# Performance work log

Hardware: AMD Instinct MI355X
Metric: run time of the kernel (lower is better)

## Reference

```python
import jax, jax.numpy as jnp
import numpy as np

EPS = 1e-6
N_HEADS = 16
KV_HEADS = 4
HEAD_DIM = 64
N_REP = N_HEADS // KV_HEADS
N_EXPERTS = 8
TOP_K = 2


def _rms_norm(x, w):
    return x * jax.lax.rsqrt(jnp.mean(x * x, axis=-1, keepdims=True) + EPS) * w


def _apply_rope(x, fc):
    # x: (B,T,H,D); fc: (T, D//2, 2) holding (cos, sin)
    B, T, H, D = x.shape
    xr = x.reshape(B, T, H, D // 2, 2)
    f = fc.reshape(1, T, 1, D // 2, 2)
    re = xr[..., 0] * f[..., 0] - xr[..., 1] * f[..., 1]
    im = xr[..., 1] * f[..., 0] + xr[..., 0] * f[..., 1]
    return jnp.stack([re, im], axis=-1).reshape(B, T, H, D)


def _silu(x):
    return x * jax.nn.sigmoid(x)


def setup_inputs():
    key = jax.random.key(0)
    ks = jax.random.split(key, 16)
    B, T, C = 4, 1024, 1024
    IE, IS = 1024, 2048  # expert_inter_dim, shared inter_dim
    s = 0.02
    x = jax.random.normal(ks[0], (B, T, C), jnp.float32)
    inv_freq = 1.0 / (10000.0 ** (np.arange(0, HEAD_DIM, 2, dtype=np.float32) / HEAD_DIM))
    ang = np.outer(np.arange(T, dtype=np.float32), inv_freq)
    freq_cis = jnp.asarray(np.stack([np.cos(ang), np.sin(ang)], axis=-1), jnp.float32)
    causal = np.tril(np.ones((T, T), dtype=bool))
    mask = jnp.asarray(np.where(causal, 0.0, -1e9), dtype=jnp.float32).reshape(1, 1, T, T)
    window = jnp.zeros((1, 1, T, T), jnp.float32)
    return {
        "x": x,
        "freq_cis": freq_cis,
        "mask": mask,
        "window": window,
        "norm1_w": jnp.ones((C,), jnp.float32),
        "wq": jax.random.normal(ks[1], (N_HEADS * HEAD_DIM, C), jnp.float32) * s,
        "wk": jax.random.normal(ks[2], (KV_HEADS * HEAD_DIM, C), jnp.float32) * s,
        "wv": jax.random.normal(ks[3], (KV_HEADS * HEAD_DIM, C), jnp.float32) * s,
        "wo": jax.random.normal(ks[4], (C, N_HEADS * HEAD_DIM), jnp.float32) * s,
        "norm2_w": jnp.ones((C,), jnp.float32),
        "gate_w": jax.random.normal(ks[5], (N_EXPERTS, C), jnp.float32) * s,
        "exp_w1": jax.random.normal(ks[6], (N_EXPERTS, IE, C), jnp.float32) * s,
        "exp_w2": jax.random.normal(ks[7], (N_EXPERTS, IE, C), jnp.float32) * s,
        "exp_wp": jax.random.normal(ks[8], (N_EXPERTS, C, IE), jnp.float32) * s,
        "sh_w1": jax.random.normal(ks[9], (IS, C), jnp.float32) * s,
        "sh_w2": jax.random.normal(ks[10], (IS, C), jnp.float32) * s,
        "sh_wp": jax.random.normal(ks[11], (C, IS), jnp.float32) * s,
        "start_pos": 0,
    }


def reference(x, freq_cis, mask, window, norm1_w, wq, wk, wv, wo, norm2_w,
              gate_w, exp_w1, exp_w2, exp_wp, sh_w1, sh_w2, sh_wp, start_pos):
    B, T, C = x.shape
    # ---- pre-norm attention (GQA, Global mask, eval: no dropout) ----
    xn = _rms_norm(x, norm1_w)
    q = (xn @ wq.T).reshape(B, T, N_HEADS, HEAD_DIM)
    k = (xn @ wk.T).reshape(B, T, KV_HEADS, HEAD_DIM)
    v = (xn @ wv.T).reshape(B, T, KV_HEADS, HEAD_DIM)
    q = _apply_rope(q, freq_cis)
    k = _apply_rope(k, freq_cis)
    k = jnp.repeat(k, N_REP, axis=2)  # (B,T,H,D)
    v = jnp.repeat(v, N_REP, axis=2)
    scale = 1.0 / np.sqrt(HEAD_DIM).astype(np.float32)
    att = jnp.einsum("bqhd,bkhd->bhqk", q, k) * scale + mask
    p = jax.nn.softmax(att, axis=-1)
    o = jnp.einsum("bhqk,bkhd->bqhd", p, v).reshape(B, T, C)
    x = x + o @ wo.T
    # ---- pre-norm MoE FFN ----
    xn2 = _rms_norm(x, norm2_w).reshape(-1, C)  # (N,C)
    scores = xn2 @ gate_w.T                      # gate logits, returned
    probs = jax.nn.softmax(scores, axis=-1)
    top_w, top_i = jax.lax.top_k(probs, TOP_K)   # (N,K)
    # dense combine weights (N,E): zero for non-selected experts
    wfull = jnp.sum(jax.nn.one_hot(top_i, N_EXPERTS, dtype=x.dtype) * top_w[..., None], axis=1)
    h = _silu(jnp.einsum("nc,eic->eni", xn2, exp_w1)) * jnp.einsum("nc,eic->eni", xn2, exp_w2)
    ye = jnp.einsum("eni,eci->enc", h, exp_wp)   # per-expert outputs
    y = jnp.einsum("ne,enc->nc", wfull, ye)      # routed combine
    z = (_silu(xn2 @ sh_w1.T) * (xn2 @ sh_w2.T)) @ sh_wp.T  # shared expert
    out = x + (y + z).reshape(B, T, C)
    return out, scores
```

## Files before the change

### kernel.cpp

```cpp
#include <hip/hip_runtime.h>


typedef __bf16 bf16_t;
typedef __bf16 bf16x8 __attribute__((ext_vector_type(8)));
typedef __bf16 bf16x4 __attribute__((ext_vector_type(4)));
typedef float  f32x4  __attribute__((ext_vector_type(4)));

#define LQKV 1536

#define GLD16(gp, lp) __builtin_amdgcn_global_load_lds(                         \
    (const __attribute__((address_space(1))) void*)(gp),                        \
    (__attribute__((address_space(3))) void*)(lp), 16, 0, 0)

__global__ __launch_bounds__(256) void convert_k(
    const float* __restrict__ src, bf16_t* __restrict__ dst)
{
    size_t i = (size_t)blockIdx.x * 256 + threadIdx.x;
    float4 v = *((const float4*)src + i);
    bf16x4 o;
    o[0] = (bf16_t)v.x; o[1] = (bf16_t)v.y; o[2] = (bf16_t)v.z; o[3] = (bf16_t)v.w;
    *((bf16x4*)dst + i) = o;
}

struct Cvt8 {
    const float* s[8];
    bf16_t* d[8];
    int cum[9];
    int nseg;
};

__global__ __launch_bounds__(256) void convert_multi_k(Cvt8 j)
{
    int blk = blockIdx.x;
    int seg = 0;
    while (seg + 1 < j.nseg && blk >= j.cum[seg + 1]) ++seg;
    size_t i = (size_t)(blk - j.cum[seg]) * 256 + threadIdx.x;
    float4 v = *((const float4*)j.s[seg] + i);
    bf16x4 o;
    o[0] = (bf16_t)v.x; o[1] = (bf16_t)v.y; o[2] = (bf16_t)v.z; o[3] = (bf16_t)v.w;
    *((bf16x4*)j.d[seg] + i) = o;
}

__global__ __launch_bounds__(256) void gemm_bt(
    const bf16_t* __restrict__ A, const bf16_t* __restrict__ W,
    int M, int N, int K, int ldw, int mode,
    float* __restrict__ outF, bf16_t* __restrict__ outB,
    const float* __restrict__ resF, float* __restrict__ outF2)
{
    __shared__ __align__(16) bf16_t sA[128 * 64];
    __shared__ __align__(16) bf16_t sB[128 * 64];
    const int tid  = threadIdx.x;
    const int bm   = blockIdx.y * 128, bn = blockIdx.x * 128;
    const int lane = tid & 63;
    const int wv   = tid >> 6;
    const int wm   = (wv >> 1) * 64, wn = (wv & 1) * 64;
    const int lr   = lane & 15;
    const int kg   = lane >> 4;

    f32x4 acc[4][4];
    #pragma unroll
    for (int i = 0; i < 4; ++i)
        #pragma unroll
        for (int j = 0; j < 4; ++j)
            acc[i][j] = f32x4{0.f, 0.f, 0.f, 0.f};

    for (int k0 = 0; k0 < K; k0 += 64) {
        #pragma unroll
        for (int p = 0; p < 4; ++p) {
            int idx = p * 256 + tid;
            int row = idx >> 3, ch = (idx & 7) * 8;
            GLD16(A + (size_t)(bm + row) * K   + k0 + ch, sA + idx * 8);
            GLD16(W + (size_t)(bn + row) * ldw + k0 + ch, sB + idx * 8);
        }
        __syncthreads();
        #pragma unroll
        for (int ks = 0; ks < 2; ++ks) {
            bf16x8 af[4], bfr[4];
            #pragma unroll
            for (int i = 0; i < 4; ++i)
                af[i] = *(const bf16x8*)(sA + (wm + i * 16 + lr) * 64 + ks * 32 + kg * 8);
            #pragma unroll
            for (int j = 0; j < 4; ++j)
                bfr[j] = *(const bf16x8*)(sB + (wn + j * 16 + lr) * 64 + ks * 32 + kg * 8);
            #pragma unroll
            for (int i = 0; i < 4; ++i)
                #pragma unroll
                for (int j = 0; j < 4; ++j)
                    acc[i][j] = __builtin_amdgcn_mfma_f32_16x16x32_bf16(
                        af[i], bfr[j], acc[i][j], 0, 0, 0);
        }
        __syncthreads();
    }

    #pragma unroll
    for (int i = 0; i < 4; ++i) {
        #pragma unroll
        for (int j = 0; j < 4; ++j) {
            #pragma unroll
            for (int rr = 0; rr < 4; ++rr) {
                int m = bm + wm + i * 16 + kg * 4 + rr;
                int n = bn + wn + j * 16 + lr;
                size_t o = (size_t)m * N + n;
                float v = acc[i][j][rr];
                if (mode == 0)      outF[o] = v;
                else if (mode == 1) outB[o] = (bf16_t)v;
                else if (mode == 2) {
                    float r = v + resF[o];
                    outF[o] = r;
                    if (outF2) outF2[o] = r;
                } else              outF[o] += v;
            }
        }
    }
}

__global__ __launch_bounds__(256) void gemm_glu(
    const bf16_t* __restrict__ A, const bf16_t* __restrict__ W1,
    const bf16_t* __restrict__ W2, int M, int N, int K,
    bf16_t* __restrict__ out)
{
    __shared__ __align__(16) bf16_t sA[128 * 64];
    __shared__ __align__(16) bf16_t sB1[128 * 64];
    __shared__ __align__(16) bf16_t sB2[128 * 64];
    const int tid  = threadIdx.x;
    const int bm   = blockIdx.y * 128, bn = blockIdx.x * 128;
    const int lane = tid & 63;
    const int wv   = tid >> 6;
    const int wm   = (wv >> 1) * 64, wn = (wv & 1) * 64;
    const int lr   = lane & 15;
    const int kg   = lane >> 4;

    f32x4 acc1[4][4], acc2[4][4];
    #pragma unroll
    for (int i = 0; i < 4; ++i)
        #pragma unroll
        for (int j = 0; j < 4; ++j) {
            acc1[i][j] = f32x4{0.f, 0.f, 0.f, 0.f};
            acc2[i][j] = f32x4{0.f, 0.f, 0.f, 0.f};
        }

    for (int k0 = 0; k0 < K; k0 += 64) {
        #pragma unroll
        for (int p = 0; p < 4; ++p) {
            int idx = p * 256 + tid;
            int row = idx >> 3, ch = (idx & 7) * 8;
            GLD16(A  + (size_t)(bm + row) * K + k0 + ch, sA  + idx * 8);
            GLD16(W1 + (size_t)(bn + row) * K + k0 + ch, sB1 + idx * 8);
            GLD16(W2 + (size_t)(bn + row) * K + k0 + ch, sB2 + idx * 8);
        }
        __syncthreads();
        #pragma unroll
        for (int ks = 0; ks < 2; ++ks) {
            bf16x8 af[4], b1[4], b2[4];
            #pragma unroll
            for (int i = 0; i < 4; ++i)
                af[i] = *(const bf16x8*)(sA + (wm + i * 16 + lr) * 64 + ks * 32 + kg * 8);
            #pragma unroll
            for (int j = 0; j < 4; ++j) {
                b1[j] = *(const bf16x8*)(sB1 + (wn + j * 16 + lr) * 64 + ks * 32 + kg * 8);
                b2[j] = *(const bf16x8*)(sB2 + (wn + j * 16 + lr) * 64 + ks * 32 + kg * 8);
            }
            #pragma unroll
            for (int i = 0; i < 4; ++i)
                #pragma unroll
                for (int j = 0; j < 4; ++j) {
                    acc1[i][j] = __builtin_amdgcn_mfma_f32_16x16x32_bf16(
                        af[i], b1[j], acc1[i][j], 0, 0, 0);
                    acc2[i][j] = __builtin_amdgcn_mfma_f32_16x16x32_bf16(
                        af[i], b2[j], acc2[i][j], 0, 0, 0);
                }
        }
        __syncthreads();
    }

    #pragma unroll
    for (int i = 0; i < 4; ++i) {
        #pragma unroll
        for (int j = 0; j < 4; ++j) {
            #pragma unroll
            for (int rr = 0; rr < 4; ++rr) {
                int m = bm + wm + i * 16 + kg * 4 + rr;
                int n = bn + wn + j * 16 + lr;
                float v1 = acc1[i][j][rr], v2 = acc2[i][j][rr];
                out[(size_t)m * N + n] = (bf16_t)(v1 / (1.f + __expf(-v1)) * v2);
            }
        }
    }
}

__device__ __forceinline__ int seg_off(const int* cnt, int e)
{
    int r = 0;
    #pragma unroll
    for (int k = 0; k < 8; ++k) if (k < e) r += (cnt[k] + 127) & ~127;
    return r;
}

__global__ __launch_bounds__(256) void glu_gather(
    const bf16_t* __restrict__ A, const bf16_t* __restrict__ W1,
    const bf16_t* __restrict__ W2, const int* __restrict__ tok_list,
    const int* __restrict__ cnt, bf16_t* __restrict__ h)
{
    const int e = blockIdx.y >> 5, t = blockIdx.y & 31;
    const int ce = cnt[e];
    if (t * 128 >= ce) return;
    const int hbase = seg_off(cnt, e) + t * 128;
    const bf16_t* W1e = W1 + (size_t)e * 1048576;
    const bf16_t* W2e = W2 + (size_t)e * 1048576;

    __shared__ __align__(16) bf16_t sA[128 * 64];
    __shared__ __align__(16) bf16_t sB1[128 * 64];
    __shared__ __align__(16) bf16_t sB2[128 * 64];
    const int tid  = threadIdx.x;
    const int bn   = blockIdx.x * 128;
    const int lane = tid & 63;
    const int wv   = tid >> 6;
    const int wm   = (wv >> 1) * 64, wn = (wv & 1) * 64;
    const int lr   = lane & 15;
    const int kg   = lane >> 4;

    int tok4[4];
    #pragma unroll
    for (int p = 0; p < 4; ++p)
        tok4[p] = tok_list[e * 4096 + t * 128 + ((p * 256 + tid) >> 3)];

    f32x4 acc1[4][4], acc2[4][4];
    #pragma unroll
    for (int i = 0; i < 4; ++i)
        #pragma unroll
        for (int j = 0; j < 4; ++j) {
            acc1[i][j] = f32x4{0.f, 0.f, 0.f, 0.f};
            acc2[i][j] = f32x4{0.f, 0.f, 0.f, 0.f};
        }

    for (int k0 = 0; k0 < 1024; k0 += 64) {
        #pragma unroll
        for (int p = 0; p < 4; ++p) {
            int idx = p * 256 + tid;
            int row = idx >> 3, ch = (idx & 7) * 8;
            GLD16(A   + (size_t)tok4[p] * 1024 + k0 + ch,    sA  + idx * 8);
            GLD16(W1e + (size_t)(bn + row) * 1024 + k0 + ch, sB1 + idx * 8);
            GLD16(W2e + (size_t)(bn + row) * 1024 + k0 + ch, sB2 + idx * 8);
        }
        __syncthreads();
        #pragma unroll
        for (int ks = 0; ks < 2; ++ks) {
            bf16x8 af[4], b1[4], b2[4];
            #pragma unroll
            for (int i = 0; i < 4; ++i)
                af[i] = *(const bf16x8*)(sA + (wm + i * 16 + lr) * 64 + ks * 32 + kg * 8);
            #pragma unroll
            for (int j = 0; j < 4; ++j) {
                b1[j] = *(const bf16x8*)(sB1 + (wn + j * 16 + lr) * 64 + ks * 32 + kg * 8);
                b2[j] = *(const bf16x8*)(sB2 + (wn + j * 16 + lr) * 64 + ks * 32 + kg * 8);
            }
            #pragma unroll
            for (int i = 0; i < 4; ++i)
                #pragma unroll
                for (int j = 0; j < 4; ++j) {
                    acc1[i][j] = __builtin_amdgcn_mfma_f32_16x16x32_bf16(
                        af[i], b1[j], acc1[i][j], 0, 0, 0);
                    acc2[i][j] = __builtin_amdgcn_mfma_f32_16x16x32_bf16(
                        af[i], b2[j], acc2[i][j], 0, 0, 0);
                }
        }
        __syncthreads();
    }

    #pragma unroll
    for (int i = 0; i < 4; ++i) {
        #pragma unroll
        for (int j = 0; j < 4; ++j) {
            #pragma unroll
            for (int rr = 0; rr < 4; ++rr) {
                int rl = wm + i * 16 + kg * 4 + rr;
                int n  = bn + wn + j * 16 + lr;
                float v1 = acc1[i][j][rr], v2 = acc2[i][j][rr];
                h[(size_t)(hbase + rl) * 1024 + n] =
                    (bf16_t)(v1 / (1.f + __expf(-v1)) * v2);
            }
        }
    }
}

__global__ __launch_bounds__(256) void down_gather(
    const bf16_t* __restrict__ h, const bf16_t* __restrict__ Wp,
    const int* __restrict__ tok_list, const float* __restrict__ w_list,
    const int* __restrict__ cnt, float* __restrict__ out)
{
    const int e = blockIdx.y >> 5, t = blockIdx.y & 31;
    const int ce = cnt[e];
    if (t * 128 >= ce) return;
    const int hbase = seg_off(cnt, e) + t * 128;
    const bf16_t* We = Wp + (size_t)e * 1048576;

    __shared__ __align__(16) bf16_t sA[128 * 64];
    __shared__ __align__(16) bf16_t sB[128 * 64];
    const int tid  = threadIdx.x;
    const int bn   = blockIdx.x * 128;
    const int lane = tid & 63;
    const int wv   = tid >> 6;
    const int wm   = (wv >> 1) * 64, wn = (wv & 1) * 64;
    const int lr   = lane & 15;
    const int kg   = lane >> 4;

    f32x4 acc[4][4];
    #pragma unroll
    for (int i = 0; i < 4; ++i)
        #pragma unroll
        for (int j = 0; j < 4; ++j)
            acc[i][j] = f32x4{0.f, 0.f, 0.f, 0.f};

    for (int k0 = 0; k0 < 1024; k0 += 64) {
        #pragma unroll
        for (int p = 0; p < 4; ++p) {
            int idx = p * 256 + tid;
            int row = idx >> 3, ch = (idx & 7) * 8;
            GLD16(h  + (size_t)(hbase + row) * 1024 + k0 + ch, sA + idx * 8);
            GLD16(We + (size_t)(bn + row) * 1024 + k0 + ch,    sB + idx * 8);
        }
        __syncthreads();
        #pragma unroll
        for (int ks = 0; ks < 2; ++ks) {
            bf16x8 af[4], bfr[4];
            #pragma unroll
            for (int i = 0; i < 4; ++i)
                af[i] = *(const bf16x8*)(sA + (wm + i * 16 + lr) * 64 + ks * 32 + kg * 8);
            #pragma unroll
            for (int j = 0; j < 4; ++j)
                bfr[j] = *(const bf16x8*)(sB + (wn + j * 16 + lr) * 64 + ks * 32 + kg * 8);
            #pragma unroll
            for (int i = 0; i < 4; ++i)
                #pragma unroll
                for (int j = 0; j < 4; ++j)
                    acc[i][j] = __builtin_amdgcn_mfma_f32_16x16x32_bf16(
                        af[i], bfr[j], acc[i][j], 0, 0, 0);
        }
        __syncthreads();
    }

    #pragma unroll
    for (int i = 0; i < 4; ++i) {
        #pragma unroll
        for (int rr = 0; rr < 4; ++rr) {
            int g = t * 128 + wm + i * 16 + kg * 4 + rr;
            if (g < ce) {
                int   tok = tok_list[e * 4096 + g];
                float wgt = w_list[e * 4096 + g];
                #pragma unroll
                for (int j = 0; j < 4; ++j) {
                    int n = bn + wn + j * 16 + lr;
                    atomicAdd(&out[(size_t)tok * 1024 + n], wgt * acc[i][j][rr]);
                }
            }
        }
    }
}

__global__ __launch_bounds__(256) void rmsnorm_k(
    const float* __restrict__ src, const float* __restrict__ w,
    bf16_t* __restrict__ dst)
{
    const int row = blockIdx.x, tid = threadIdx.x;
    float4 t4 = *((const float4*)src + (size_t)row * 256 + tid);
    float ssum = t4.x*t4.x + t4.y*t4.y + t4.z*t4.z + t4.w*t4.w;
    #pragma unroll
    for (int off = 32; off > 0; off >>= 1) ssum += __shfl_down(ssum, off);
    __shared__ float red[4];
    if ((tid & 63) == 0) red[tid >> 6] = ssum;
    __syncthreads();
    float total = red[0] + red[1] + red[2] + red[3];
    float rms = rsqrtf(total * (1.0f / 1024.0f) + 1e-6f);
    float4 w4 = *((const float4*)w + tid);
    bf16x4 o4;
    o4[0] = (bf16_t)(t4.x * rms * w4.x);
    o4[1] = (bf16_t)(t4.y * rms * w4.y);
    o4[2] = (bf16_t)(t4.z * rms * w4.z);
    o4[3] = (bf16_t)(t4.w * rms * w4.w);
    *((bf16x4*)dst + (size_t)row * 256 + tid) = o4;
}

__global__ __launch_bounds__(256) void rmsnorm_gate_k(
    const float* __restrict__ src, const float* __restrict__ w,
    const float* __restrict__ gw, bf16_t* __restrict__ dst,
    float* __restrict__ scores, int* __restrict__ topi,
    float* __restrict__ topw)
{
    const int row = blockIdx.x, tid = threadIdx.x;
    float4 t4 = *((const float4*)src + (size_t)row * 256 + tid);
    float ssum = t4.x*t4.x + t4.y*t4.y + t4.z*t4.z + t4.w*t4.w;
    #pragma unroll
    for (int off = 32; off > 0; off >>= 1) ssum += __shfl_down(ssum, off);
    __shared__ float red[4];
    if ((tid & 63) == 0) red[tid >> 6] = ssum;
    __syncthreads();
    float total = red[0] + red[1] + red[2] + red[3];
    float rms = rsqrtf(total * (1.0f / 1024.0f) + 1e-6f);
    float4 w4 = *((const float4*)w + tid);
    float4 f4;
    f4.x = t4.x * rms * w4.x;
    f4.y = t4.y * rms * w4.y;
    f4.z = t4.z * rms * w4.z;
    f4.w = t4.w * rms * w4.w;
    bf16x4 o4;
    o4[0] = (bf16_t)f4.x; o4[1] = (bf16_t)f4.y;
    o4[2] = (bf16_t)f4.z; o4[3] = (bf16_t)f4.w;
    *((bf16x4*)dst + (size_t)row * 256 + tid) = o4;

    float a[8];
    #pragma unroll
    for (int e = 0; e < 8; ++e) {
        float4 g4 = *((const float4*)(gw + (size_t)e * 1024) + tid);
        a[e] = f4.x * g4.x + f4.y * g4.y + f4.z * g4.z + f4.w * g4.w;
    }
    #pragma unroll
    for (int e = 0; e < 8; ++e)
        #pragma unroll
        for (int off = 32; off > 0; off >>= 1) a[e] += __shfl_down(a[e], off);
    __shared__ float gred[4][8];
    if ((tid & 63) == 0)
        #pragma unroll
        for (int e = 0; e < 8; ++e) gred[tid >> 6][e] = a[e];
    __syncthreads();
    if (tid == 0) {
        float lg[8];
        #pragma unroll
        for (int e = 0; e < 8; ++e)
            lg[e] = gred[0][e] + gred[1][e] + gred[2][e] + gred[3][e];
        #pragma unroll
        for (int e = 0; e < 8; ++e) scores[(size_t)row * 8 + e] = lg[e];
        float mx = lg[0];
        #pragma unroll
        for (int e = 1; e < 8; ++e) mx = fmaxf(mx, lg[e]);
        float p[8], sum = 0.f;
        #pragma unroll
        for (int e = 0; e < 8; ++e) { p[e] = __expf(lg[e] - mx); sum += p[e]; }
        float inv = 1.0f / sum;
        #pragma unroll
        for (int e = 0; e < 8; ++e) p[e] *= inv;
        int i1 = 0;
        #pragma unroll
        for (int e = 1; e < 8; ++e) if (p[e] > p[i1]) i1 = e;
        int i2 = (i1 == 0) ? 1 : 0;
        #pragma unroll
        for (int e = 0; e < 8; ++e) if (e != i1 && p[e] > p[i2]) i2 = e;
        topi[row] = i1 | (i2 << 8);
        topw[row * 2]     = p[i1];
        topw[row * 2 + 1] = p[i2];
    }
}

__global__ __launch_bounds__(256) void build_lists_k(
    const int* __restrict__ topi, const float* __restrict__ topw,
    int* __restrict__ tok_list, float* __restrict__ w_list,
    int* __restrict__ cnt)
{
    const int e = blockIdx.x;
    const int tid = threadIdx.x, lane = tid & 63, wv = tid >> 6;
    __shared__ int wc[4];
    int base = 0;
    for (int t0 = 0; t0 < 4096; t0 += 256) {
        int tok = t0 + tid;
        int ti = topi[tok];
        int i1 = ti & 255, i2 = (ti >> 8) & 255;
        bool m = (i1 == e) || (i2 == e);
        unsigned long long b = __ballot(m);
        if (lane == 0) wc[wv] = __popcll(b);
        __syncthreads();
        int pos = base;
        #pragma unroll
        for (int k = 0; k < 4; ++k) if (k < wv) pos += wc[k];
        pos += __popcll(b & ((1ull << lane) - 1ull));
        if (m) {
            tok_list[e * 4096 + pos] = tok;
            w_list[e * 4096 + pos]   = (i1 == e) ? topw[tok * 2] : topw[tok * 2 + 1];
        }
        base += wc[0] + wc[1] + wc[2] + wc[3];
        __syncthreads();
    }
    int padded = (base + 127) & ~127;
    for (int p = base + tid; p < padded; p += 256) tok_list[e * 4096 + p] = 0;
    if (tid == 0) cnt[e] = base;
}

__global__ __launch_bounds__(256) void rope_all_k(
    bf16_t* __restrict__ qkv, const float* __restrict__ fc)
{
    int idx = blockIdx.x * 256 + threadIdx.x;
    int pr = idx & 31;
    int hn = idx >> 5;
    int h  = hn % 20;
    int n  = hn / 20;
    int tpos = n & 1023;
    const float* f = fc + ((size_t)tpos * 32 + pr) * 2;
    float c = f[0], s = f[1];
    int col = (h < 16) ? h * 64 : 1024 + (h - 16) * 64;
    size_t base = (size_t)n * LQKV + col + pr * 2;
    float x0 = (float)qkv[base], x1 = (float)qkv[base + 1];
    qkv[base]     = (bf16_t)(x0 * c - x1 * s);
    qkv[base + 1] = (bf16_t)(x1 * c + x0 * s);
}

__global__ __launch_bounds__(256) void transpose_v(
    const bf16_t* __restrict__ qkv, bf16_t* __restrict__ vt)
{
    __shared__ bf16_t tile[64][72];
    const int tt = blockIdx.x, kvh = blockIdx.y, b = blockIdx.z;
    const int tid = threadIdx.x;
    {
        int r = tid >> 2, c = (tid & 3) * 16;
        const bf16_t* src = qkv + ((size_t)(b * 1024 + tt * 64 + r)) * LQKV
                            + 1280 + kvh * 64 + c;
        bf16x8 v0 = *(const bf16x8*)src;
        bf16x8 v1 = *(const bf16x8*)(src + 8);
        *(bf16x8*)&tile[r][c] = v0;
        *(bf16x8*)&tile[r][c + 8] = v1;
    }
    __syncthreads();
    {
        int d = tid >> 2, t4 = (tid & 3) * 16;
        bf16_t* dst = vt + ((size_t)((b * 4 + kvh) * 64 + d)) * 1024 + tt * 64 + t4;
        bf16x8 o0, o1;
        #pragma unroll
        for (int u = 0; u < 8; ++u) {
            o0[u] = tile[t4 + u][d];
            o1[u] = tile[t4 + 8 + u][d];
        }
        *(bf16x8*)dst = o0;
        *(bf16x8*)(dst + 8) = o1;
    }
}

__global__ __launch_bounds__(256) void attn_mfma(
    const bf16_t* __restrict__ qkv, const bf16_t* __restrict__ vt,
    bf16_t* __restrict__ ob)
{
    const int qt = blockIdx.x, h = blockIdx.y, b = blockIdx.z;
    const int kvh = h >> 2;
    __shared__ __align__(16) bf16_t sK[64 * 64];
    __shared__ __align__(16) bf16_t sVt[64 * 64];
    __shared__ __align__(16) bf16_t sP[64 * 72];
    const int tid  = threadIdx.x;
    const int w    = tid >> 6;
    const int lane = tid & 63;
    const int lr   = lane & 15;
    const int kg   = lane >> 4;
    const int swz  = (lr & 7) << 3;

    bf16x8 qf[2];
    {
        const bf16_t* qrow = qkv + ((size_t)(b * 1024 + qt * 64 + w * 16 + lr)) * LQKV
                             + h * 64;
        qf[0] = *(const bf16x8*)(qrow + kg * 8);
        qf[1] = *(const bf16x8*)(qrow + 32 + kg * 8);
    }
    float m_run[4], l_run[4];
    f32x4 o_acc[4];
    #pragma unroll
    for (int rr = 0; rr < 4; ++rr) { m_run[rr] = -1.0e30f; l_run[rr] = 0.f; }
    #pragma unroll
    for (int dt = 0; dt < 4; ++dt) o_acc[dt] = f32x4{0.f, 0.f, 0.f, 0.f};

    for (int kt = 0; kt <= qt; ++kt) {
        #pragma unroll
        for (int p = 0; p < 2; ++p) {
            int idx = p * 256 + tid;
            int row = idx >> 3;
            int chs = ((idx & 7) * 8) ^ ((row & 7) << 3);
            GLD16(qkv + ((size_t)(b * 1024 + kt * 64 + row)) * LQKV
                      + 1024 + kvh * 64 + chs, sK + idx * 8);
            GLD16(vt + ((size_t)((b * 4 + kvh) * 64 + row)) * 1024 + kt * 64 + chs,
                  sVt + idx * 8);
        }
        __syncthreads();

        f32x4 sfr[4];
        #pragma unroll
        for (int j = 0; j < 4; ++j) {
            sfr[j] = f32x4{0.f, 0.f, 0.f, 0.f};
            #pragma unroll
            for (int ks = 0; ks < 2; ++ks) {
                bf16x8 bf = *(const bf16x8*)(sK + (j * 16 + lr) * 64 +
                                             ((ks * 32 + kg * 8) ^ swz));
                sfr[j] = __builtin_amdgcn_mfma_f32_16x16x32_bf16(qf[ks], bf, sfr[j], 0, 0, 0);
            }
        }
        const int rowg = qt * 64 + w * 16 + kg * 4;
        float mnew[4];
        #pragma unroll
        for (int rr = 0; rr < 4; ++rr) mnew[rr] = m_run[rr];
        #pragma unroll
        for (int j = 0; j < 4; ++j) {
            int colg = kt * 64 + j * 16 + lr;
            #pragma unroll
            for (int rr = 0; rr < 4; ++rr) {
                float s = sfr[j][rr] * 0.125f;
                if (colg > rowg + rr) s = -1.0e30f;
                sfr[j][rr] = s;
                mnew[rr] = fmaxf(mnew[rr], s);
            }
        }
        #pragma unroll
        for (int off = 1; off < 16; off <<= 1)
            #pragma unroll
            for (int rr = 0; rr < 4; ++rr)
                mnew[rr] = fmaxf(mnew[rr], __shfl_xor(mnew[rr], off, 64));
        float alpha[4], lpart[4];
        #pragma unroll
        for (int rr = 0; rr < 4; ++rr) {
            alpha[rr] = __expf(m_run[rr] - mnew[rr]);
            lpart[rr] = 0.f;
        }
        #pragma unroll
        for (int j = 0; j < 4; ++j)
            #pragma unroll
            for (int rr = 0; rr < 4; ++rr) {
                float p = __expf(sfr[j][rr] - mnew[rr]);
                sfr[j][rr] = p;
                lpart[rr] += p;
            }
        #pragma unroll
        for (int j = 0; j < 4; ++j)
            #pragma unroll
            for (int rr = 0; rr < 4; ++rr)
                sP[(w * 16 + kg * 4 + rr) * 72 + j * 16 + lr] = (bf16_t)sfr[j][rr];
        #pragma unroll
        for (int off = 1; off < 16; off <<= 1)
            #pragma unroll
            for (int rr = 0; rr < 4; ++rr)
                lpart[rr] += __shfl_xor(lpart[rr], off, 64);
        #pragma unroll
        for (int rr = 0; rr < 4; ++rr) {
            l_run[rr] = l_run[rr] * alpha[rr] + lpart[rr];
            m_run[rr] = mnew[rr];
        }
        #pragma unroll
        for (int dt = 0; dt < 4; ++dt)
            #pragma unroll
            for (int rr = 0; rr < 4; ++rr)
                o_acc[dt][rr] *= alpha[rr];
        #pragma unroll
        for (int ks = 0; ks < 2; ++ks) {
            bf16x8 af = *(const bf16x8*)(sP + (w * 16 + lr) * 72 + ks * 32 + kg * 8);
            #pragma unroll
            for (int dt = 0; dt < 4; ++dt) {
                bf16x8 bf = *(const bf16x8*)(sVt + (dt * 16 + lr) * 64 +
                                             ((ks * 32 + kg * 8) ^ swz));
                o_acc[dt] = __builtin_amdgcn_mfma_f32_16x16x32_bf16(af, bf, o_acc[dt], 0, 0, 0);
            }
        }
        __syncthreads();
    }

    float inv[4];
    #pragma unroll
    for (int rr = 0; rr < 4; ++rr) inv[rr] = 1.0f / l_run[rr];
    #pragma unroll
    for (int dt = 0; dt < 4; ++dt)
        #pragma unroll
        for (int rr = 0; rr < 4; ++rr) {
            int tok = qt * 64 + w * 16 + kg * 4 + rr;
            ob[((size_t)(b * 1024 + tok)) * 1024 + h * 64 + dt * 16 + lr] =
                (bf16_t)(o_acc[dt][rr] * inv[rr]);
        }
}

extern "C" void kernel_launch(void* const* d_in, const int* in_sizes, int n_in,
                              void* d_out, int out_size, void* d_ws, size_t ws_size,
                              hipStream_t stream)
{
    const float* x   = (const float*)d_in[0];
    const float* fc  = (const float*)d_in[1];
    const float* n1w = (const float*)d_in[4];
    const float* wq  = (const float*)d_in[5];
    const float* wk  = (const float*)d_in[6];
    const float* wv  = (const float*)d_in[7];
    const float* wo  = (const float*)d_in[8];
    const float* n2w = (const float*)d_in[9];
    const float* gw  = (const float*)d_in[10];
    const float* ew1 = (const float*)d_in[11];
    const float* ew2 = (const float*)d_in[12];
    const float* ewp = (const float*)d_in[13];
    const float* sw1 = (const float*)d_in[14];
    const float* sw2 = (const float*)d_in[15];
    const float* swp = (const float*)d_in[16];

    const size_t MB = 1024 * 1024;
    char* ws = (char*)d_ws;
    bf16_t* xnb  = (bf16_t*)(ws + 0);
    float*  x1   = (float*) (ws + 8 * MB);
    bf16_t* ew2b = (bf16_t*)(ws + 8 * MB);
    bf16_t* h    = (bf16_t*)(ws + 24 * MB);
    char*   lists= ws + 42 * MB;
    int*    tok_list = (int*)lists;
    float*  w_list   = (float*)(lists + 131072);
    int*    cnt      = (int*)(lists + 262144);
    int*    topi     = (int*)(lists + 262400);
    float*  topw     = (float*)(lists + 278784);
    bf16_t* sw1b = (bf16_t*)(ws + 43 * MB);
    bf16_t* sw2b = (bf16_t*)(ws + 47 * MB);
    bf16_t* swpb = (bf16_t*)(ws + 51 * MB);
    char*   slotA= ws + 55 * MB;
    bf16_t* hb   = (bf16_t*)slotA;
    bf16_t* qkv  = (bf16_t*)(ws + 71 * MB);
    bf16_t* ob   = (bf16_t*)(ws + 83 * MB);
    bf16_t* vt   = (bf16_t*)(ws + 91 * MB);
    bf16_t* ew1b = (bf16_t*)(ws + 71 * MB);
    bf16_t* ewpb = (bf16_t*)(ws + 71 * MB);

    float* outp   = (float*)d_out;
    float* scores = outp + (size_t)4096 * 1024;

    auto gemm = [&](const bf16_t* A, const bf16_t* W, int M, int N, int K, int ldw,
                    int mode, float* oF, bf16_t* oB, const float* res, float* oF2) {
        gemm_bt<<<dim3(N / 128, M / 128), 256, 0, stream>>>(
            A, W, M, N, K, ldw, mode, oF, oB, res, oF2);
    };

    bf16_t* wqb = (bf16_t*)slotA;
    bf16_t* wkb = wqb + 1048576;
    bf16_t* wvb = wkb + 262144;
    bf16_t* wob = wvb + 262144;
    {
        Cvt8 j;
        j.s[0]=wq;  j.d[0]=wqb;  j.s[1]=wk;  j.d[1]=wkb;
        j.s[2]=wv;  j.d[2]=wvb;  j.s[3]=wo;  j.d[3]=wob;
        j.s[4]=sw1; j.d[4]=sw1b; j.s[5]=sw2; j.d[5]=sw2b;
        j.s[6]=swp; j.d[6]=swpb; j.s[7]=nullptr; j.d[7]=nullptr;
        int sz[7] = {1024, 256, 256, 1024, 2048, 2048, 2048};
        j.cum[0] = 0;
        for (int k = 0; k < 7; ++k) j.cum[k + 1] = j.cum[k] + sz[k];
        j.cum[8] = j.cum[7];
        j.nseg = 7;
        convert_multi_k<<<j.cum[7], 256, 0, stream>>>(j);
    }

    rmsnorm_k<<<4096, 256, 0, stream>>>(x, n1w, xnb);
    gemm(xnb, wqb, 4096, LQKV, 1024, 1024, 1, nullptr, qkv, nullptr, nullptr);
    rope_all_k<<<(4096 * 20 * 32) / 256, 256, 0, stream>>>(qkv, fc);
    transpose_v<<<dim3(16, 4, 4), 256, 0, stream>>>(qkv, vt);
    attn_mfma<<<dim3(16, 16, 4), 256, 0, stream>>>(qkv, vt, ob);
    gemm(ob, wob, 4096, 1024, 1024, 1024, 2, x1, nullptr, x, outp);

    rmsnorm_gate_k<<<4096, 256, 0, stream>>>(x1, n2w, gw, xnb, scores, topi, topw);
    build_lists_k<<<8, 256, 0, stream>>>(topi, topw, tok_list, w_list, cnt);

    {
        Cvt8 j;
        j.s[0]=ew1; j.d[0]=ew1b; j.s[1]=ew2; j.d[1]=ew2b;
        for (int k = 2; k < 8; ++k) { j.s[k]=nullptr; j.d[k]=nullptr; }
        j.cum[0] = 0; j.cum[1] = 8192; j.cum[2] = 16384;
        for (int k = 3; k < 9; ++k) j.cum[k] = 16384;
        j.nseg = 2;
        convert_multi_k<<<16384, 256, 0, stream>>>(j);
    }

    gemm_glu<<<dim3(16, 32), 256, 0, stream>>>(xnb, sw1b, sw2b, 4096, 2048, 1024, hb);
    glu_gather<<<dim3(8, 256), 256, 0, stream>>>(xnb, ew1b, ew2b, tok_list, cnt, h);

    convert_k<<<8192, 256, 0, stream>>>(ewp, ewpb);

    gemm(hb, swpb, 4096, 1024, 2048, 2048, 3, outp, nullptr, nullptr, nullptr);
    down_gather<<<dim3(8, 256), 256, 0, stream>>>(h, ewpb, tok_list, w_list, cnt, outp);

    (void)in_sizes; (void)n_in; (void)out_size; (void)ws_size;
}
```

Measured before the change: 675.1 us.

## Double-buffer LDS tiles and XOR-swizzle layout in all GEMM kernels

Converts the four MFMA GEMM kernels (gemm_bt, gemm_glu, glu_gather, down_gather) from single-buffered to double-buffered LDS. The next K-tile is issued with global_load_lds while MFMAs run on the current tile, and one vmcnt-wait plus barrier per iteration replaces the two __syncthreads. It also applies an XOR swizzle on the 8-element chunk index, keyed by row, to both the LDS writes and reads to cut bank conflicts. This doubles LDS use per block (the GLU kernels go to 96KB), which may lower occupancy.

```diff
diff --git a/kernel.cpp b/kernel.cpp
--- a/kernel.cpp
+++ b/kernel.cpp
@@ -11,6 +11,11 @@
 #define GLD16(gp, lp) __builtin_amdgcn_global_load_lds(                         \
     (const __attribute__((address_space(1))) void*)(gp),                        \
     (__attribute__((address_space(3))) void*)(lp), 16, 0, 0)
+
+#define PIPE_BARRIER() do {                                                     \
+    asm volatile("s_waitcnt vmcnt(0)" ::: "memory");                            \
+    __builtin_amdgcn_s_barrier();                                               \
+} while (0)
 
 __global__ __launch_bounds__(256) void convert_k(
     const float* __restrict__ src, bf16_t* __restrict__ dst)
@@ -47,8 +52,8 @@
     float* __restrict__ outF, bf16_t* __restrict__ outB,
     const float* __restrict__ resF, float* __restrict__ outF2)
 {
-    __shared__ __align__(16) bf16_t sA[128 * 64];
-    __shared__ __align__(16) bf16_t sB[128 * 64];
+    __shared__ __align__(16) bf16_t sA[2][128 * 64];
+    __shared__ __align__(16) bf16_t sB[2][128 * 64];
     const int tid  = threadIdx.x;
     const int bm   = blockIdx.y * 128, bn = blockIdx.x * 128;
     const int lane = tid & 63;
@@ -56,6 +61,7 @@
     const int wm   = (wv >> 1) * 64, wn = (wv & 1) * 64;
     const int lr   = lane & 15;
     const int kg   = lane >> 4;
+    const int swz  = (lr & 7) << 3;
 
     f32x4 acc[4][4];
     #pragma unroll
@@ -64,24 +70,33 @@
         for (int j = 0; j < 4; ++j)
             acc[i][j] = f32x4{0.f, 0.f, 0.f, 0.f};
 
-    for (int k0 = 0; k0 < K; k0 += 64) {
+    auto STAGE = [&](int b, int k0) {
         #pragma unroll
         for (int p = 0; p < 4; ++p) {
             int idx = p * 256 + tid;
-            int row = idx >> 3, ch = (idx & 7) * 8;
-            GLD16(A + (size_t)(bm + row) * K   + k0 + ch, sA + idx * 8);
-            GLD16(W + (size_t)(bn + row) * ldw + k0 + ch, sB + idx * 8);
-        }
-        __syncthreads();
+            int row = idx >> 3;
+            int ch  = ((idx & 7) * 8) ^ ((row & 7) << 3);
+            GLD16(A + (size_t)(bm + row) * K   + k0 + ch, sA[b] + idx * 8);
+            GLD16(W + (size_t)(bn + row) * ldw + k0 + ch, sB[b] + idx * 8);
+        }
+    };
+
+    STAGE(0, 0);
+    PIPE_BARRIER();
+    int cur = 0;
+    for (int k0 = 0; k0 < K; k0 += 64) {
+        if (k0 + 64 < K) STAGE(cur ^ 1, k0 + 64);
         #pragma unroll
         for (int ks = 0; ks < 2; ++ks) {
             bf16x8 af[4], bfr[4];
             #pragma unroll
             for (int i = 0; i < 4; ++i)
-                af[i] = *(const bf16x8*)(sA + (wm + i * 16 + lr) * 64 + ks * 32 + kg * 8);
+                af[i] = *(const bf16x8*)(sA[cur] + (wm + i * 16 + lr) * 64 +
+                                         ((ks * 32 + kg * 8) ^ swz));
             #pragma unroll
             for (int j = 0; j < 4; ++j)
-                bfr[j] = *(const bf16x8*)(sB + (wn + j * 16 + lr) * 64 + ks * 32 + kg * 8);
+                bfr[j] = *(const bf16x8*)(sB[cur] + (wn + j * 16 + lr) * 64 +
+                                          ((ks * 32 + kg * 8) ^ swz));
             #pragma unroll
             for (int i = 0; i < 4; ++i)
                 #pragma unroll
@@ -89,7 +104,8 @@
                     acc[i][j] = __builtin_amdgcn_mfma_f32_16x16x32_bf16(
                         af[i], bfr[j], acc[i][j], 0, 0, 0);
         }
-        __syncthreads();
+        PIPE_BARRIER();
+        cur ^= 1;
     }
 
     #pragma unroll
@@ -119,9 +135,9 @@
     const bf16_t* __restrict__ W2, int M, int N, int K,
     bf16_t* __restrict__ out)
 {
-    __shared__ __align__(16) bf16_t sA[128 * 64];
-    __shared__ __align__(16) bf16_t sB1[128 * 64];
-    __shared__ __align__(16) bf16_t sB2[128 * 64];
+    __shared__ __align__(16) bf16_t sA[2][128 * 64];
+    __shared__ __align__(16) bf16_t sB1[2][128 * 64];
+    __shared__ __align__(16) bf16_t sB2[2][128 * 64];
     const int tid  = threadIdx.x;
     const int bm   = blockIdx.y * 128, bn = blockIdx.x * 128;
     const int lane = tid & 63;
@@ -129,6 +145,7 @@
     const int wm   = (wv >> 1) * 64, wn = (wv & 1) * 64;
     const int lr   = lane & 15;
     const int kg   = lane >> 4;
+    const int swz  = (lr & 7) << 3;
 
     f32x4 acc1[4][4], acc2[4][4];
     #pragma unroll
@@ -139,26 +156,36 @@
             acc2[i][j] = f32x4{0.f, 0.f, 0.f, 0.f};
         }
 
-    for (int k0 = 0; k0 < K; k0 += 64) {
+    auto STAGE = [&](int b, int k0) {
         #pragma unroll
         for (int p = 0; p < 4; ++p) {
             int idx = p * 256 + tid;
-            int row = idx >> 3, ch = (idx & 7) * 8;
-            GLD16(A  + (size_t)(bm + row) * K + k0 + ch, sA  + idx * 8);
-            GLD16(W1 + (size_t)(bn + row) * K + k0 + ch, sB1 + idx * 8);
-            GLD16(W2 + (size_t)(bn + row) * K + k0 + ch, sB2 + idx * 8);
-        }
-        __syncthreads();
+            int row = idx >> 3;
+            int ch  = ((idx & 7) * 8) ^ ((row & 7) << 3);
+            GLD16(A  + (size_t)(bm + row) * K + k0 + ch, sA[b]  + idx * 8);
+            GLD16(W1 + (size_t)(bn + row) * K + k0 + ch, sB1[b] + idx * 8);
+            GLD16(W2 + (size_t)(bn + row) * K + k0 + ch, sB2[b] + idx * 8);
+        }
+    };
+
+    STAGE(0, 0);
+    PIPE_BARRIER();
+    int cur = 0;
+    for (int k0 = 0; k0 < K; k0 += 64) {
+        if (k0 + 64 < K) STAGE(cur ^ 1, k0 + 64);
         #pragma unroll
         for (int ks = 0; ks < 2; ++ks) {
             bf16x8 af[4], b1[4], b2[4];
             #pragma unroll
             for (int i = 0; i < 4; ++i)
-                af[i] = *(const bf16x8*)(sA + (wm + i * 16 + lr) * 64 + ks * 32 + kg * 8);
+                af[i] = *(const bf16x8*)(sA[cur] + (wm + i * 16 + lr) * 64 +
+                                         ((ks * 32 + kg * 8) ^ swz));
             #pragma unroll
             for (int j = 0; j < 4; ++j) {
-                b1[j] = *(const bf16x8*)(sB1 + (wn + j * 16 + lr) * 64 + ks * 32 + kg * 8);
-                b2[j] = *(const bf16x8*)(sB2 + (wn + j * 16 + lr) * 64 + ks * 32 + kg * 8);
+                b1[j] = *(const bf16x8*)(sB1[cur] + (wn + j * 16 + lr) * 64 +
+                                         ((ks * 32 + kg * 8) ^ swz));
+                b2[j] = *(const bf16x8*)(sB2[cur] + (wn + j * 16 + lr) * 64 +
+                                         ((ks * 32 + kg * 8) ^ swz));
             }
             #pragma unroll
             for (int i = 0; i < 4; ++i)
@@ -170,7 +197,8 @@
                         af[i], b2[j], acc2[i][j], 0, 0, 0);
                 }
         }
-        __syncthreads();
+        PIPE_BARRIER();
+        cur ^= 1;
     }
 
     #pragma unroll
@@ -208,9 +236,9 @@
     const bf16_t* W1e = W1 + (size_t)e * 1048576;
     const bf16_t* W2e = W2 + (size_t)e * 1048576;
 
-    __shared__ __align__(16) bf16_t sA[128 * 64];
-    __shared__ __align__(16) bf16_t sB1[128 * 64];
-    __shared__ __align__(16) bf16_t sB2[128 * 64];
+    __shared__ __align__(16) bf16_t sA[2][128 * 64];
+    __shared__ __align__(16) bf16_t sB1[2][128 * 64];
+    __shared__ __align__(16) bf16_t sB2[2][128 * 64];
     const int tid  = threadIdx.x;
     const int bn   = blockIdx.x * 128;
     const int lane = tid & 63;
@@ -218,6 +246,7 @@
     const int wm   = (wv >> 1) * 64, wn = (wv & 1) * 64;
     const int lr   = lane & 15;
     const int kg   = lane >> 4;
+    const int swz  = (lr & 7) << 3;
 
     int tok4[4];
     #pragma unroll
@@ -233,26 +262,36 @@
             acc2[i][j] = f32x4{0.f, 0.f, 0.f, 0.f};
         }
 
-    for (int k0 = 0; k0 < 1024; k0 += 64) {
+    auto STAGE = [&](int b, int k0) {
         #pragma unroll
         for (int p = 0; p < 4; ++p) {
             int idx = p * 256 + tid;
-            int row = idx >> 3, ch = (idx & 7) * 8;
-            GLD16(A   + (size_t)tok4[p] * 1024 + k0 + ch,    sA  + idx * 8);
-            GLD16(W1e + (size_t)(bn + row) * 1024 + k0 + ch, sB1 + idx * 8);
-            GLD16(W2e + (size_t)(bn + row) * 1024 + k0 + ch, sB2 + idx * 8);
-        }
-        __syncthreads();
+            int row = idx >> 3;
+            int ch  = ((idx & 7) * 8) ^ ((row & 7) << 3);
+            GLD16(A   + (size_t)tok4[p] * 1024 + k0 + ch,    sA[b]  + idx * 8);
+            GLD16(W1e + (size_t)(bn + row) * 1024 + k0 + ch, sB1[b] + idx * 8);
+            GLD16(W2e + (size_t)(bn + row) * 1024 + k0 + ch, sB2[b] + idx * 8);
+        }
+    };
+
+    STAGE(0, 0);
+    PIPE_BARRIER();
+    int cur = 0;
+    for (int k0 = 0; k0 < 1024; k0 += 64) {
+        if (k0 + 64 < 1024) STAGE(cur ^ 1, k0 + 64);
         #pragma unroll
         for (int ks = 0; ks < 2; ++ks) {
             bf16x8 af[4], b1[4], b2[4];
             #pragma unroll
             for (int i = 0; i < 4; ++i)
-                af[i] = *(const bf16x8*)(sA + (wm + i * 16 + lr) * 64 + ks * 32 + kg * 8);
+                af[i] = *(const bf16x8*)(sA[cur] + (wm + i * 16 + lr) * 64 +
+                                         ((ks * 32 + kg * 8) ^ swz));
             #pragma unroll
             for (int j = 0; j < 4; ++j) {
-                b1[j] = *(const bf16x8*)(sB1 + (wn + j * 16 + lr) * 64 + ks * 32 + kg * 8);
-                b2[j] = *(const bf16x8*)(sB2 + (wn + j * 16 + lr) * 64 + ks * 32 + kg * 8);
+                b1[j] = *(const bf16x8*)(sB1[cur] + (wn + j * 16 + lr) * 64 +
+                                         ((ks * 32 + kg * 8) ^ swz));
+                b2[j] = *(const bf16x8*)(sB2[cur] + (wn + j * 16 + lr) * 64 +
+                                         ((ks * 32 + kg * 8) ^ swz));
             }
             #pragma unroll
             for (int i = 0; i < 4; ++i)
@@ -264,7 +303,8 @@
                         af[i], b2[j], acc2[i][j], 0, 0, 0);
                 }
         }
-        __syncthreads();
+        PIPE_BARRIER();
+        cur ^= 1;
     }
 
     #pragma unroll
@@ -294,8 +334,8 @@
     const int hbase = seg_off(cnt, e) + t * 128;
     const bf16_t* We = Wp + (size_t)e * 1048576;
 
-    __shared__ __align__(16) bf16_t sA[128 * 64];
-    __shared__ __align__(16) bf16_t sB[128 * 64];
+    __shared__ __align__(16) bf16_t sA[2][128 * 64];
+    __shared__ __align__(16) bf16_t sB[2][128 * 64];
     const int tid  = threadIdx.x;
     const int bn   = blockIdx.x * 128;
     const int lane = tid & 63;
@@ -303,6 +343,7 @@
     const int wm   = (wv >> 1) * 64, wn = (wv & 1) * 64;
     const int lr   = lane & 15;
     const int kg   = lane >> 4;
+    const int swz  = (lr & 7) << 3;
 
     f32x4 acc[4][4];
     #pragma unroll
@@ -311,24 +352,33 @@
         for (int j = 0; j < 4; ++j)
             acc[i][j] = f32x4{0.f, 0.f, 0.f, 0.f};
 
-    for (int k0 = 0; k0 < 1024; k0 += 64) {
+    auto STAGE = [&](int b, int k0) {
         #pragma unroll
         for (int p = 0; p < 4; ++p) {
             int idx = p * 256 + tid;
-            int row = idx >> 3, ch = (idx & 7) * 8;
-            GLD16(h  + (size_t)(hbase + row) * 1024 + k0 + ch, sA + idx * 8);
-            GLD16(We + (size_t)(bn + row) * 1024 + k0 + ch,    sB + idx * 8);
-        }
-        __syncthreads();
+            int row = idx >> 3;
+            int ch  = ((idx & 7) * 8) ^ ((row & 7) << 3);
+            GLD16(h  + (size_t)(hbase + row) * 1024 + k0 + ch, sA[b] + idx * 8);
+            GLD16(We + (size_t)(bn + row) * 1024 + k0 + ch,    sB[b] + idx * 8);
+        }
+    };
+
+    STAGE(0, 0);
+    PIPE_BARRIER();
+    int cur = 0;
+    for (int k0 = 0; k0 < 1024; k0 += 64) {
+        if (k0 + 64 < 1024) STAGE(cur ^ 1, k0 + 64);
         #pragma unroll
         for (int ks = 0; ks < 2; ++ks) {
             bf16x8 af[4], bfr[4];
             #pragma unroll
             for (int i = 0; i < 4; ++i)
-                af[i] = *(const bf16x8*)(sA + (wm + i * 16 + lr) * 64 + ks * 32 + kg * 8);
+                af[i] = *(const bf16x8*)(sA[cur] + (wm + i * 16 + lr) * 64 +
+                                         ((ks * 32 + kg * 8) ^ swz));
             #pragma unroll
             for (int j = 0; j < 4; ++j)
-                bfr[j] = *(const bf16x8*)(sB + (wn + j * 16 + lr) * 64 + ks * 32 + kg * 8);
+                bfr[j] = *(const bf16x8*)(sB[cur] + (wn + j * 16 + lr) * 64 +
+                                          ((ks * 32 + kg * 8) ^ swz));
             #pragma unroll
             for (int i = 0; i < 4; ++i)
                 #pragma unroll
@@ -336,7 +386,8 @@
                     acc[i][j] = __builtin_amdgcn_mfma_f32_16x16x32_bf16(
                         af[i], bfr[j], acc[i][j], 0, 0, 0);
         }
-        __syncthreads();
+        PIPE_BARRIER();
+        cur ^= 1;
     }
 
     #pragma unroll
```

Result: faster. 617.5 us (-8.5%).
